# Kernel tuning notes

Hardware: AMD Instinct MI355X
Metric: run time of the kernel (lower is better)

Reference implementation:

```python
import jax, jax.numpy as jnp
import numpy as np

B, N, D, U = 128, 1024, 16, 128


def setup_inputs() -> dict:
    key = jax.random.key(0)
    ks = jax.random.split(key, 12)
    # get_normalized_adj: D^{-1/2} (A + I) D^{-1/2} on a sparse random graph
    A = (jax.random.uniform(ks[0], (N, N)) < 0.01).astype(jnp.float32)
    A = A + jnp.eye(N, dtype=jnp.float32)
    dinv = 1.0 / jnp.sqrt(A.sum(axis=1))
    support = dinv[:, None] * A * dinv[None, :]
    s = 0.05
    return {
        "x": jax.random.normal(ks[1], (2, B, N, D), jnp.float32),
        "hx": jax.random.normal(ks[2], (B, N * U), jnp.float32),
        "delta": jax.random.normal(ks[3], (B, N, D), jnp.float32),
        "support": support,
        "kernel_r": jax.random.normal(ks[4], (D + U, 2 * U), jnp.float32) * jnp.sqrt(2.0 / (D + U)),
        "kernel_c": jax.random.normal(ks[5], (D + U, U), jnp.float32) * jnp.sqrt(2.0 / (D + U)),
        "w_out": jax.random.normal(ks[6], (U + D, D), jnp.float32) * s,
        "b_out": jax.random.normal(ks[7], (D,), jnp.float32) * s,
        "w_basis": jax.random.normal(ks[8], (D, D), jnp.float32) * s,
        "b_basis": jax.random.normal(ks[9], (D,), jnp.float32) * s,
        "lam": jax.random.normal(ks[10], (1,), jnp.float32),
    }


def reference(x, hx, delta, support, kernel_r, kernel_c, w_out, b_out, w_basis, b_basis, lam):
    y_basis, y_res = x[0], x[1]                       # (B, N, D) each
    # speculative delta (add=True branch)
    delta_value = jax.nn.relu(y_res @ w_basis + b_basis)
    p_t = jax.nn.sigmoid(y_res + 0.5 * jnp.sqrt(jnp.abs(delta + 1e-9)))
    new_delta = lam * (2.0 * p_t - 1.0) * delta_value  # (B, N, D)

    hx3 = hx.reshape(B, N, U)

    def gconv(inp, state, kernel):
        # inp (B,N,D), state (B,N,U); diffusion_step == 1 Chebyshev pass
        xs = jnp.concatenate([inp, state], axis=-1)      # (B, N, D+U)
        xs = jnp.einsum('ij,bjl->bil', support, xs)      # diffusion over nodes
        return xs @ kernel                               # (B, N, out)

    value = jax.nn.sigmoid(gconv(y_basis, hx3, kernel_r))  # (B, N, 2U)
    r, u = value[..., :U], value[..., U:]
    c = jnp.tanh(gconv(y_basis, r * hx3, kernel_c))        # (B, N, U)

    u_flat = u.reshape(B, N * U)
    c_flat = c.reshape(B, N * U)
    new_state = hx * u_flat + c_flat * (1.0 - u_flat)      # (B, N*U)

    concat = jnp.concatenate([new_state.reshape(B, N, U), y_basis], axis=-1)
    o = concat @ w_out + b_out + new_delta                 # (B, N, D)
    return (o, new_state, new_delta)
```

## Files before the change

kernel.cpp:

```cpp
#include <hip/hip_runtime.h>
#include <cstdint>

#define B_ 128
#define N_ 1024
#define D_ 16
#define U_ 128
#define M_ (B_*N_)
#define K_ 144
#define KP 192
#define CAP 48

typedef unsigned short u16;
typedef unsigned int   u32;
typedef __attribute__((ext_vector_type(8))) short bf16x8;
typedef __attribute__((ext_vector_type(4))) float f32x4;

__device__ __forceinline__ float bf2f(u16 h){ return __uint_as_float(((u32)h) << 16); }
__device__ __forceinline__ u16 f2bf(float f){
    u32 u = __float_as_uint(f);
    return (u16)((u + 0x7FFFu + ((u >> 16) & 1u)) >> 16);
}
__device__ __forceinline__ float sig_(float x){ return 1.0f / (1.0f + __expf(-x)); }

__global__ void k_ell(const float* __restrict__ sup, float* __restrict__ vals,
                      int* __restrict__ cols, int* __restrict__ nnz)
{
    int wid  = (blockIdx.x * blockDim.x + threadIdx.x) >> 6;
    int lane = threadIdx.x & 63;
    if (wid >= N_) return;
    const float* row = sup + (size_t)wid * N_;
    int base = 0;
    for (int step = 0; step < N_/64; ++step){
        int j = step*64 + lane;
        float v = row[j];
        unsigned long long m = __ballot(v != 0.0f);
        int pos = base + __popcll(m & ((1ull << lane) - 1ull));
        if (v != 0.0f && pos < CAP){ vals[wid*CAP + pos] = v; cols[wid*CAP + pos] = j; }
        base += __popcll(m);
    }
    int cnt = base < CAP ? base : CAP;
    for (int p = cnt + lane; p < CAP; p += 64){
        vals[wid*CAP + p] = 0.0f;
        cols[wid*CAP + p] = 0;
    }
    if (lane == 0) nnz[wid] = (cnt + 3) & ~3;
}

__global__ void k_prep(const float* __restrict__ kr, const float* __restrict__ kc,
                       u16* __restrict__ wr_t, u16* __restrict__ wc_t)
{
    int t = blockIdx.x * 256 + threadIdx.x;
    if (t < 256*KP){
        int col = t / KP, k = t % KP;
        wr_t[t] = f2bf(k < K_ ? kr[k*256 + col] : 0.0f);
    } else {
        int q = t - 256*KP;
        int col = q / KP, k = q % KP;
        wc_t[q] = f2bf(k < K_ ? kc[k*128 + col] : 0.0f);
    }
}


#define GQ(JJ, WW)                                                             \
    {   float4 h = s4[(int)(JJ)*4 + (cq ^ ((int)(JJ) & 3))];                   \
        acc.x = fmaf((WW), h.x, acc.x); acc.y = fmaf((WW), h.y, acc.y);        \
        acc.z = fmaf((WW), h.z, acc.z); acc.w = fmaf((WW), h.w, acc.w); }

#define GB(T0)                                                                 \
    {   float4 wv = *(const float4*)(vt + (T0));                               \
        int4   jv = *(const int4*)(ct + (T0));                                 \
        GQ(jv.x, wv.x); GQ(jv.y, wv.y); GQ(jv.z, wv.z); GQ(jv.w, wv.w); }

__global__ __launch_bounds__(512, 4) void k_spmm1(
        const float* __restrict__ x, const float* __restrict__ hx,
        const float* __restrict__ vals, const int* __restrict__ cols,
        const int* __restrict__ nnz, u16* __restrict__ agg)
{
    __shared__ float s_hx[1024*16];
    const int chunk = blockIdx.x;
    const int b     = blockIdx.y;
    const int tid   = threadIdx.x;
    float4* s4 = (float4*)s_hx;

    if (chunk >= 9){
        int cb = 144 + (chunk - 9) * 16;
        uint4 z = {0,0,0,0};
        for (int p = tid; p < 2048; p += 512){
            int node = p >> 1, half = p & 1;
            size_t m = (size_t)(b<<10) + node;
            *(uint4*)&agg[m*KP + cb + half*8] = z;
        }
        return;
    }

    const int cb = chunk * 16;
    for (int q = tid; q < 4096; q += 512){
        int row = q >> 2, qi = q & 3;
        int xscol = cb + qi*4;
        float4 v;
        if (xscol < 16)
            v = *(const float4*)&x[((size_t)((b<<10)+row))*16 + xscol];
        else
            v = *(const float4*)&hx[((size_t)((b<<10)+row))*128 + (xscol-16)];
        s4[row*4 + (qi ^ (row & 3))] = v;
    }
    __syncthreads();

    for (int p = tid; p < 4096; p += 512){
        int node = p >> 2, cq = p & 3;
        int c = nnz[node];
        const float* vt = vals + node*CAP;
        const int*   ct = cols + node*CAP;
        float4 acc = make_float4(0.f,0.f,0.f,0.f);
        GB(0) GB(4) GB(8) GB(12)
        for (int t0 = 16; t0 < c; t0 += 4) GB(t0)
        size_t m = (size_t)(b<<10) + node;
        ushort4 pv; pv.x = f2bf(acc.x); pv.y = f2bf(acc.y);
        pv.z = f2bf(acc.z); pv.w = f2bf(acc.w);
        *(ushort4*)&agg[m*KP + cb + cq*4] = pv;
    }
}

__global__ __launch_bounds__(512, 4) void k_spmm2(
        const u16* __restrict__ value, const float* __restrict__ hx,
        const float* __restrict__ vals, const int* __restrict__ cols,
        const int* __restrict__ nnz, u16* __restrict__ agg)
{
    __shared__ float s_hx[1024*16];
    const int chunk = blockIdx.x;
    const int b     = blockIdx.y;
    const int tid   = threadIdx.x;
    const int cb    = chunk * 16;
    float4* s4 = (float4*)s_hx;

    for (int q = tid; q < 4096; q += 512){
        int row = q >> 2, qi = q & 3;
        int hxcol = cb + qi*4;
        size_t nb = (size_t)((b<<10)+row);
        float4 h = *(const float4*)&hx[nb*128 + hxcol];
        ushort4 rv = *(const ushort4*)&value[nb*256 + hxcol];
        float4 v = make_float4(bf2f(rv.x)*h.x, bf2f(rv.y)*h.y,
                               bf2f(rv.z)*h.z, bf2f(rv.w)*h.w);
        s4[row*4 + (qi ^ (row & 3))] = v;
    }
    __syncthreads();

    for (int p = tid; p < 4096; p += 512){
        int node = p >> 2, cq = p & 3;
        int c = nnz[node];
        const float* vt = vals + node*CAP;
        const int*   ct = cols + node*CAP;
        float4 acc = make_float4(0.f,0.f,0.f,0.f);
        GB(0) GB(4) GB(8) GB(12)
        for (int t0 = 16; t0 < c; t0 += 4) GB(t0)
        size_t m = (size_t)(b<<10) + node;
        ushort4 pv; pv.x = f2bf(acc.x); pv.y = f2bf(acc.y);
        pv.z = f2bf(acc.z); pv.w = f2bf(acc.w);
        *(ushort4*)&agg[m*KP + D_ + cb + cq*4] = pv;
    }
}


#define GEMM_STAGE(DST, SRC, BASE)                                             \
    _Pragma("unroll")                                                          \
    for (int i = 0; i < 4; ++i){                                               \
        int q = tid + i*256;                                                   \
        int r_ = q >> 3, sl = q & 7;                                           \
        uint4 v = *(const uint4*)((SRC) + (size_t)((BASE)+r_)*KP + kb + sl*8); \
        *(uint4*)((DST) + r_*72 + sl*8) = v;                                   \
    }

#define GEMM_CORE                                                              \
    for (int kb = 0; kb < KP; kb += 64){                                       \
        __syncthreads();                                                       \
        GEMM_STAGE(a_s, agg, rb)                                               \
        GEMM_STAGE(w_s, wt, cb)                                                \
        __syncthreads();                                                       \
        _Pragma("unroll")                                                      \
        for (int ks = 0; ks < 2; ++ks){                                        \
            bf16x8 af[4], bfv[4];                                              \
            _Pragma("unroll")                                                  \
            for (int f = 0; f < 4; ++f){                                       \
                af[f]  = *(const bf16x8*)(a_s + (wr + f*16 + lrow)*72 + ks*32 + lk); \
                bfv[f] = *(const bf16x8*)(w_s + (wc + f*16 + lrow)*72 + ks*32 + lk); \
            }                                                                  \
            _Pragma("unroll")                                                  \
            for (int fr = 0; fr < 4; ++fr)                                     \
                _Pragma("unroll")                                              \
                for (int fc = 0; fc < 4; ++fc)                                 \
                    acc[fr][fc] = __builtin_amdgcn_mfma_f32_16x16x32_bf16(     \
                        af[fr], bfv[fc], acc[fr][fc], 0, 0, 0);                \
        }                                                                      \
    }

__global__ __launch_bounds__(256) void k_gemm1(const u16* __restrict__ agg,
        const u16* __restrict__ wt, u16* __restrict__ value)
{
    __shared__ u16 a_s[128*72];
    __shared__ u16 w_s[128*72];
    const int rb = blockIdx.x * 128, cb = blockIdx.y * 128;
    const int tid = threadIdx.x;
    const int wid = tid >> 6, lane = tid & 63;
    const int wr = (wid >> 1) * 64, wc = (wid & 1) * 64;
    const int lrow = lane & 15, lk = (lane >> 4) * 8;
    f32x4 acc[4][4] = {};
    GEMM_CORE
    const int rg = (lane >> 4) * 4;
    #pragma unroll
    for (int fr = 0; fr < 4; ++fr)
        #pragma unroll
        for (int fc = 0; fc < 4; ++fc)
            #pragma unroll
            for (int j = 0; j < 4; ++j){
                int row = rb + wr + fr*16 + rg + j;
                int col = cb + wc + fc*16 + lrow;
                value[(size_t)row*256 + col] = f2bf(sig_(acc[fr][fc][j]));
            }
}

__global__ __launch_bounds__(256) void k_gemm2(const u16* __restrict__ agg,
        const u16* __restrict__ wt, const float* __restrict__ hx,
        const u16* value, float* ns_out)
{
    __shared__ u16 a_s[128*72];
    __shared__ u16 w_s[128*72];
    const int rb = blockIdx.x * 128, cb = 0;
    const int tid = threadIdx.x;
    const int wid = tid >> 6, lane = tid & 63;
    const int wr = (wid >> 1) * 64, wc = (wid & 1) * 64;
    const int lrow = lane & 15, lk = (lane >> 4) * 8;
    f32x4 acc[4][4] = {};
    GEMM_CORE
    const int rg = (lane >> 4) * 4;
    float ov[4][4][4];
    #pragma unroll
    for (int fr = 0; fr < 4; ++fr)
        #pragma unroll
        for (int fc = 0; fc < 4; ++fc)
            #pragma unroll
            for (int j = 0; j < 4; ++j){
                int row = rb + wr + fr*16 + rg + j;
                int col = wc + fc*16 + lrow;
                float u = bf2f(value[(size_t)row*256 + 128 + col]);
                float h = hx[(size_t)row*128 + col];
                float c = tanhf(acc[fr][fc][j]);
                ov[fr][fc][j] = h*u + c*(1.0f - u);
            }
    __syncthreads();
    #pragma unroll
    for (int fr = 0; fr < 4; ++fr)
        #pragma unroll
        for (int fc = 0; fc < 4; ++fc)
            #pragma unroll
            for (int j = 0; j < 4; ++j){
                int row = rb + wr + fr*16 + rg + j;
                int col = wc + fc*16 + lrow;
                ns_out[(size_t)row*128 + col] = ov[fr][fc][j];
            }
}

__global__ __launch_bounds__(256) void k_out(const float* __restrict__ ns,
        const float* __restrict__ x, const float* __restrict__ delta,
        const float* __restrict__ wo, const float* __restrict__ bo,
        const float* __restrict__ wb, const float* __restrict__ bb,
        const float* __restrict__ lam,
        float* __restrict__ o, float* __restrict__ nd_out)
{
    __shared__ float ns_s[64][132];
    __shared__ float yb_s[64][20];
    __shared__ float yr_s[64][20];
    __shared__ float w_s[144][16];
    __shared__ float wb_s[16][16];
    __shared__ float bo_s[16], bb_s[16];
    int rowbase = blockIdx.x * 64;
    int tid = threadIdx.x;
    const float* yr = x + (size_t)M_ * D_;
    #pragma unroll
    for (int jj = 0; jj < 8; ++jj){
        int q = tid + 256*jj;
        int row = q >> 5, c4 = (q & 31) * 4;
        *(float4*)&ns_s[row][c4] = *(const float4*)&ns[(size_t)(rowbase + row)*U_ + c4];
    }
    {
        int row = tid >> 2, c4 = (tid & 3) * 4;
        *(float4*)&yb_s[row][c4] = *(const float4*)&x[(size_t)(rowbase + row)*D_ + c4];
        *(float4*)&yr_s[row][c4] = *(const float4*)&yr[(size_t)(rowbase + row)*D_ + c4];
    }
    #pragma unroll
    for (int jj = 0; jj < 3; ++jj){
        int q = tid + 256*jj;
        if (q < 576){ int k = q >> 2, d4 = (q & 3) * 4;
            *(float4*)&w_s[k][d4] = *(const float4*)&wo[k*D_ + d4]; }
    }
    wb_s[tid >> 4][tid & 15] = wb[tid];
    if (tid < 16){ bo_s[tid] = bo[tid]; bb_s[tid] = bb[tid]; }
    __syncthreads();
    int row = tid >> 2, d0 = (tid & 3) * 4;
    float4 acc = make_float4(0.f,0.f,0.f,0.f);
    for (int k = 0; k < U_; ++k){
        float cs = ns_s[row][k];
        float4 w = *(const float4*)&w_s[k][d0];
        acc.x = fmaf(cs, w.x, acc.x); acc.y = fmaf(cs, w.y, acc.y);
        acc.z = fmaf(cs, w.z, acc.z); acc.w = fmaf(cs, w.w, acc.w);
    }
    #pragma unroll
    for (int k = 0; k < D_; ++k){
        float cs = yb_s[row][k];
        float4 w = *(const float4*)&w_s[U_ + k][d0];
        acc.x = fmaf(cs, w.x, acc.x); acc.y = fmaf(cs, w.y, acc.y);
        acc.z = fmaf(cs, w.z, acc.z); acc.w = fmaf(cs, w.w, acc.w);
    }
    float4 dacc = make_float4(bb_s[d0], bb_s[d0+1], bb_s[d0+2], bb_s[d0+3]);
    #pragma unroll
    for (int k = 0; k < D_; ++k){
        float yv = yr_s[row][k];
        float4 w = *(const float4*)&wb_s[k][d0];
        dacc.x = fmaf(yv, w.x, dacc.x); dacc.y = fmaf(yv, w.y, dacc.y);
        dacc.z = fmaf(yv, w.z, dacc.z); dacc.w = fmaf(yv, w.w, dacc.w);
    }
    size_t off = (size_t)(rowbase + row)*D_ + d0;
    float4 dl = *(const float4*)&delta[off];
    float lm = lam[0];
    float nd4[4];
    float yv4[4] = {yr_s[row][d0], yr_s[row][d0+1], yr_s[row][d0+2], yr_s[row][d0+3]};
    float dv4[4] = {fmaxf(dacc.x,0.f), fmaxf(dacc.y,0.f), fmaxf(dacc.z,0.f), fmaxf(dacc.w,0.f)};
    float dl4[4] = {dl.x, dl.y, dl.z, dl.w};
    #pragma unroll
    for (int j = 0; j < 4; ++j){
        float pt = sig_(yv4[j] + 0.5f * sqrtf(fabsf(dl4[j] + 1e-9f)));
        nd4[j] = lm * (2.0f * pt - 1.0f) * dv4[j];
    }
    float4 bov = *(const float4*)&bo_s[d0];
    float4 ov = make_float4(acc.x + bov.x + nd4[0], acc.y + bov.y + nd4[1],
                            acc.z + bov.z + nd4[2], acc.w + bov.w + nd4[3]);
    *(float4*)&nd_out[off] = make_float4(nd4[0], nd4[1], nd4[2], nd4[3]);
    *(float4*)&o[off] = ov;
}

extern "C" void kernel_launch(void* const* d_in, const int* in_sizes, int n_in,
                              void* d_out, int out_size, void* d_ws, size_t ws_size,
                              hipStream_t stream)
{
    const float* x        = (const float*)d_in[0];
    const float* hx       = (const float*)d_in[1];
    const float* delta    = (const float*)d_in[2];
    const float* support  = (const float*)d_in[3];
    const float* kernel_r = (const float*)d_in[4];
    const float* kernel_c = (const float*)d_in[5];
    const float* w_out    = (const float*)d_in[6];
    const float* b_out    = (const float*)d_in[7];
    const float* w_basis  = (const float*)d_in[8];
    const float* b_basis  = (const float*)d_in[9];
    const float* lam      = (const float*)d_in[10];

    float* out = (float*)d_out;
    float* o   = out;
    float* ns  = out + 2097152;
    float* nd  = out + 18874368;
    u16*   value = (u16*)ns;

    char* ws = (char*)d_ws;
    float* ell_vals = (float*)ws;
    int*   ell_cols = (int*)(ws + 1024*CAP*4);
    int*   ell_nnz  = (int*)(ws + 2*1024*CAP*4);
    u16*   agg      = (u16*)(ws + (1 << 20));
    u16*   wr_t     = (u16*)(ws + (1 << 20) + (size_t)M_*KP*2);
    u16*   wc_t     = wr_t + 256*KP;

    k_ell  <<<256, 256, 0, stream>>>(support, ell_vals, ell_cols, ell_nnz);
    k_prep <<<(256*KP + 128*KP)/256, 256, 0, stream>>>(kernel_r, kernel_c, wr_t, wc_t);
    k_spmm1<<<dim3(12,128), 512, 0, stream>>>(x, hx, ell_vals, ell_cols, ell_nnz, agg);
    k_gemm1<<<dim3(M_/128, 2), 256, 0, stream>>>(agg, wr_t, value);
    k_spmm2<<<dim3(8,128), 512, 0, stream>>>(value, hx, ell_vals, ell_cols, ell_nnz, agg);
    k_gemm2<<<M_/128, 256, 0, stream>>>(agg, wc_t, hx, value, ns);
    k_out  <<<M_/64, 256, 0, stream>>>(ns, x, delta, w_out, b_out,
                                       w_basis, b_basis, lam, o, nd);
}
```

Measured before the change: 237.4 us.

## Stage SpMM node features as bf16 in LDS and drop padding-zero pass

```diff
diff --git a/kernel.cpp b/kernel.cpp
--- a/kernel.cpp
+++ b/kernel.cpp
@@ -61,48 +61,46 @@
 }
 
 
-#define GQ(JJ, WW)                                                             \
-    {   float4 h = s4[(int)(JJ)*4 + (cq ^ ((int)(JJ) & 3))];                   \
-        acc.x = fmaf((WW), h.x, acc.x); acc.y = fmaf((WW), h.y, acc.y);        \
-        acc.z = fmaf((WW), h.z, acc.z); acc.w = fmaf((WW), h.w, acc.w); }
+#define GQB(JJ, WW)                                                            \
+    {   uint2 hh = *(const uint2*)(s16 + (int)(JJ)*16 + cq*4);                 \
+        float f0 = __uint_as_float(hh.x << 16);                                \
+        float f1 = __uint_as_float(hh.x & 0xFFFF0000u);                        \
+        float f2 = __uint_as_float(hh.y << 16);                                \
+        float f3 = __uint_as_float(hh.y & 0xFFFF0000u);                        \
+        acc.x = fmaf((WW), f0, acc.x); acc.y = fmaf((WW), f1, acc.y);          \
+        acc.z = fmaf((WW), f2, acc.z); acc.w = fmaf((WW), f3, acc.w); }
 
 #define GB(T0)                                                                 \
     {   float4 wv = *(const float4*)(vt + (T0));                               \
         int4   jv = *(const int4*)(ct + (T0));                                 \
-        GQ(jv.x, wv.x); GQ(jv.y, wv.y); GQ(jv.z, wv.z); GQ(jv.w, wv.w); }
-
-__global__ __launch_bounds__(512, 4) void k_spmm1(
+        GQB(jv.x, wv.x); GQB(jv.y, wv.y); GQB(jv.z, wv.z); GQB(jv.w, wv.w); }
+
+#define PACK8(PK, VA, VB)                                                      \
+    uint4 PK; PK.x = (u32)f2bf((VA).x) | ((u32)f2bf((VA).y) << 16);            \
+    PK.y = (u32)f2bf((VA).z) | ((u32)f2bf((VA).w) << 16);                      \
+    PK.z = (u32)f2bf((VB).x) | ((u32)f2bf((VB).y) << 16);                      \
+    PK.w = (u32)f2bf((VB).z) | ((u32)f2bf((VB).w) << 16);
+
+__global__ __launch_bounds__(512, 8) void k_spmm1(
         const float* __restrict__ x, const float* __restrict__ hx,
         const float* __restrict__ vals, const int* __restrict__ cols,
         const int* __restrict__ nnz, u16* __restrict__ agg)
 {
-    __shared__ float s_hx[1024*16];
+    __shared__ u16 s16[1024*16];
     const int chunk = blockIdx.x;
     const int b     = blockIdx.y;
     const int tid   = threadIdx.x;
-    float4* s4 = (float4*)s_hx;
-
-    if (chunk >= 9){
-        int cb = 144 + (chunk - 9) * 16;
-        uint4 z = {0,0,0,0};
-        for (int p = tid; p < 2048; p += 512){
-            int node = p >> 1, half = p & 1;
-            size_t m = (size_t)(b<<10) + node;
-            *(uint4*)&agg[m*KP + cb + half*8] = z;
-        }
-        return;
-    }
-
-    const int cb = chunk * 16;
-    for (int q = tid; q < 4096; q += 512){
-        int row = q >> 2, qi = q & 3;
-        int xscol = cb + qi*4;
-        float4 v;
-        if (xscol < 16)
-            v = *(const float4*)&x[((size_t)((b<<10)+row))*16 + xscol];
-        else
-            v = *(const float4*)&hx[((size_t)((b<<10)+row))*128 + (xscol-16)];
-        s4[row*4 + (qi ^ (row & 3))] = v;
+    const int cb    = chunk * 16;
+
+    for (int q = tid; q < 2048; q += 512){
+        int row = q >> 1, part = q & 1;
+        const float* src = (chunk == 0)
+            ? &x[((size_t)((b<<10)+row))*16 + part*8]
+            : &hx[((size_t)((b<<10)+row))*128 + (cb-16) + part*8];
+        float4 va = *(const float4*)src;
+        float4 vb = *(const float4*)(src + 4);
+        PACK8(pk, va, vb)
+        *(uint4*)(s16 + row*16 + part*8) = pk;
     }
     __syncthreads();
 
@@ -121,27 +119,31 @@
     }
 }
 
-__global__ __launch_bounds__(512, 4) void k_spmm2(
+__global__ __launch_bounds__(512, 8) void k_spmm2(
         const u16* __restrict__ value, const float* __restrict__ hx,
         const float* __restrict__ vals, const int* __restrict__ cols,
         const int* __restrict__ nnz, u16* __restrict__ agg)
 {
-    __shared__ float s_hx[1024*16];
+    __shared__ u16 s16[1024*16];
     const int chunk = blockIdx.x;
     const int b     = blockIdx.y;
     const int tid   = threadIdx.x;
     const int cb    = chunk * 16;
-    float4* s4 = (float4*)s_hx;
-
-    for (int q = tid; q < 4096; q += 512){
-        int row = q >> 2, qi = q & 3;
-        int hxcol = cb + qi*4;
+
+    for (int q = tid; q < 2048; q += 512){
+        int row = q >> 1, part = q & 1;
         size_t nb = (size_t)((b<<10)+row);
-        float4 h = *(const float4*)&hx[nb*128 + hxcol];
-        ushort4 rv = *(const ushort4*)&value[nb*256 + hxcol];
-        float4 v = make_float4(bf2f(rv.x)*h.x, bf2f(rv.y)*h.y,
-                               bf2f(rv.z)*h.z, bf2f(rv.w)*h.w);
-        s4[row*4 + (qi ^ (row & 3))] = v;
+        int hxcol = cb + part*8;
+        float4 h0 = *(const float4*)&hx[nb*128 + hxcol];
+        float4 h1 = *(const float4*)&hx[nb*128 + hxcol + 4];
+        ushort4 r0 = *(const ushort4*)&value[nb*256 + hxcol];
+        ushort4 r1 = *(const ushort4*)&value[nb*256 + hxcol + 4];
+        float4 va = make_float4(bf2f(r0.x)*h0.x, bf2f(r0.y)*h0.y,
+                                bf2f(r0.z)*h0.z, bf2f(r0.w)*h0.w);
+        float4 vb = make_float4(bf2f(r1.x)*h1.x, bf2f(r1.y)*h1.y,
+                                bf2f(r1.z)*h1.z, bf2f(r1.w)*h1.w);
+        PACK8(pk, va, vb)
+        *(uint4*)(s16 + row*16 + part*8) = pk;
     }
     __syncthreads();
 
@@ -161,20 +163,31 @@
 }
 
 
-#define GEMM_STAGE(DST, SRC, BASE)                                             \
+#define GEMM_STAGE_A                                                           \
     _Pragma("unroll")                                                          \
     for (int i = 0; i < 4; ++i){                                               \
         int q = tid + i*256;                                                   \
         int r_ = q >> 3, sl = q & 7;                                           \
-        uint4 v = *(const uint4*)((SRC) + (size_t)((BASE)+r_)*KP + kb + sl*8); \
-        *(uint4*)((DST) + r_*72 + sl*8) = v;                                   \
+        uint4 v = {0,0,0,0};                                                   \
+        if (kb + sl*8 < K_)                                                    \
+            v = *(const uint4*)(agg + (size_t)(rb+r_)*KP + kb + sl*8);         \
+        *(uint4*)(a_s + r_*72 + sl*8) = v;                                     \
+    }
+
+#define GEMM_STAGE_W                                                           \
+    _Pragma("unroll")                                                          \
+    for (int i = 0; i < 4; ++i){                                               \
+        int q = tid + i*256;                                                   \
+        int r_ = q >> 3, sl = q & 7;                                           \
+        uint4 v = *(const uint4*)(wt + (size_t)(cb+r_)*KP + kb + sl*8);        \
+        *(uint4*)(w_s + r_*72 + sl*8) = v;                                     \
     }
 
 #define GEMM_CORE                                                              \
     for (int kb = 0; kb < KP; kb += 64){                                       \
         __syncthreads();                                                       \
-        GEMM_STAGE(a_s, agg, rb)                                               \
-        GEMM_STAGE(w_s, wt, cb)                                                \
+        GEMM_STAGE_A                                                           \
+        GEMM_STAGE_W                                                           \
         __syncthreads();                                                       \
         _Pragma("unroll")                                                      \
         for (int ks = 0; ks < 2; ++ks){                                        \
@@ -369,7 +382,7 @@
 
     k_ell  <<<256, 256, 0, stream>>>(support, ell_vals, ell_cols, ell_nnz);
     k_prep <<<(256*KP + 128*KP)/256, 256, 0, stream>>>(kernel_r, kernel_c, wr_t, wc_t);
-    k_spmm1<<<dim3(12,128), 512, 0, stream>>>(x, hx, ell_vals, ell_cols, ell_nnz, agg);
+    k_spmm1<<<dim3(9,128), 512, 0, stream>>>(x, hx, ell_vals, ell_cols, ell_nnz, agg);
     k_gemm1<<<dim3(M_/128, 2), 256, 0, stream>>>(agg, wr_t, value);
     k_spmm2<<<dim3(8,128), 512, 0, stream>>>(value, hx, ell_vals, ell_cols, ell_nnz, agg);
     k_gemm2<<<M_/128, 256, 0, stream>>>(agg, wc_t, hx, value, ns);
```

Result: slower. 244.1 us (+2.8%).
